# Performance work log

Hardware: AMD Instinct MI355X
Metric: run time of the kernel (lower is better)

## Reference

```python
import jax, jax.numpy as jnp
import numpy as np

B, T, O, H = 64, 1000, 61, 256
IN0, IN1 = 320, 2 * H  # layer0 input = 8*40 flattened feats; layer1 input = bidirectional concat


def setup_inputs() -> dict:
    key = jax.random.key(0)
    ks = jax.random.split(key, 12)
    rn = lambda k, shape: (jax.random.normal(k, shape, dtype=jnp.float32) * 0.05)
    inp = {}
    inp["batch"] = jax.random.normal(ks[0], (B, T, 8, 40), dtype=jnp.float32)
    lengths = np.random.RandomState(0).randint(T // 2, T + 1, size=B).astype(np.int64)
    inp["lengths"] = jnp.asarray(lengths)
    # GRU params stacked over directions: [2, 3H, in], [2, 3H, H], biases [2, 3H]
    inp["w_ih_l0"] = rn(ks[1], (2, 3 * H, IN0))
    inp["w_hh_l0"] = rn(ks[2], (2, 3 * H, H))
    inp["b_ih_l0"] = rn(ks[3], (2, 3 * H))
    inp["b_hh_l0"] = rn(ks[4], (2, 3 * H))
    inp["w_ih_l1"] = rn(ks[5], (2, 3 * H, IN1))
    inp["w_hh_l1"] = rn(ks[6], (2, 3 * H, H))
    inp["b_ih_l1"] = rn(ks[7], (2, 3 * H))
    inp["b_hh_l1"] = rn(ks[8], (2, 3 * H))
    inp["fc_w"] = rn(ks[9], (O, 2 * H))
    inp["fc_b"] = rn(ks[10], (O,))
    return inp


def _gru_dir(x, w_ih, w_hh, b_ih, b_hh, reverse):
    # x: [T, B, in] -> ys: [T, B, H]; torch GRU cell semantics
    def step(h, xt):
        gi = xt @ w_ih.T + b_ih          # [B, 3H]
        gh = h @ w_hh.T + b_hh           # [B, 3H]
        i_r, i_z, i_n = jnp.split(gi, 3, axis=-1)
        h_r, h_z, h_n = jnp.split(gh, 3, axis=-1)
        r = jax.nn.sigmoid(i_r + h_r)
        z = jax.nn.sigmoid(i_z + h_z)
        n = jnp.tanh(i_n + r * h_n)
        h_new = (1.0 - z) * n + z * h
        return h_new, h_new
    h0 = jnp.zeros((x.shape[1], w_hh.shape[-1]), x.dtype)
    _, ys = jax.lax.scan(step, h0, x, reverse=reverse)
    return ys


def _bigru_layer(x, w_ih, w_hh, b_ih, b_hh):
    fwd = _gru_dir(x, w_ih[0], w_hh[0], b_ih[0], b_hh[0], reverse=False)
    bwd = _gru_dir(x, w_ih[1], w_hh[1], b_ih[1], b_hh[1], reverse=True)
    return jnp.concatenate([fwd, bwd], axis=-1)  # [T, B, 2H]


def reference(batch, lengths, w_ih_l0, w_hh_l0, b_ih_l0, b_hh_l0,
              w_ih_l1, w_hh_l1, b_ih_l1, b_hh_l1, fc_w, fc_b):
    b, t = batch.shape[0], batch.shape[1]
    x = jnp.swapaxes(batch, 2, 3).reshape(b, t, -1)   # transpose(2,3).flatten(2) -> [B,T,320]
    x = jnp.swapaxes(x, 0, 1)                          # [T, B, 320] (time-major like torch GRU)
    h1 = _bigru_layer(x, w_ih_l0, w_hh_l0, b_ih_l0, b_hh_l0)
    h2 = _bigru_layer(h1, w_ih_l1, w_hh_l1, b_ih_l1, b_hh_l1)
    out = h2 @ fc_w.T + fc_b                           # [T, B, O]
    out = jnp.swapaxes(out, 0, 1)                      # [B, T, O]
    # gather first lengths[i] timesteps of each sample, concatenated
    L = np.asarray(lengths)
    mask = np.arange(t)[None, :] < L[:, None]
    bi, ti = np.nonzero(mask)
    return out[bi, ti]                                 # [sum(lengths), O]
```

## Files before the change

### kernel.cpp

```cpp
#include <hip/hip_runtime.h>
#include <cstdint>
#include <cstddef>


typedef __attribute__((ext_vector_type(8))) __bf16 bf16x8;
typedef __attribute__((ext_vector_type(4))) float f32x4;
typedef __attribute__((ext_vector_type(4))) unsigned int u32x4;

#define AS1 __attribute__((address_space(1)))
#define AS3 __attribute__((address_space(3)))

#define LOG2E 1.44269504089f
#define SRZ  (-1.44269504089f)
#define SN   (2.88539008177f)

__device__ __forceinline__ void async_ld16(const void* g, void* l) {
  __builtin_amdgcn_global_load_lds((const AS1 unsigned int*)g,
                                   (AS3 unsigned int*)l, 16, 0, 0);
}

__device__ __forceinline__ f32x4 mfma16(u32x4 a, u32x4 b, f32x4 c) {
  return __builtin_amdgcn_mfma_f32_16x16x32_bf16(
      __builtin_bit_cast(bf16x8, a), __builtin_bit_cast(bf16x8, b), c, 0, 0, 0);
}

__device__ __forceinline__ unsigned short f2b(float f) {
  unsigned int u = __float_as_uint(f);
  u += 0x7fffu + ((u >> 16) & 1u);
  return (unsigned short)(u >> 16);
}
__device__ __forceinline__ float b2f(unsigned short s) {
  return __uint_as_float(((unsigned int)s) << 16);
}
__device__ __forceinline__ float gload(const float* p, size_t i) { return p[i]; }
__device__ __forceinline__ float gload(const unsigned short* p, size_t i) { return b2f(p[i]); }
__device__ __forceinline__ void gstore(float* p, size_t i, float v) { p[i] = v; }
__device__ __forceinline__ void gstore(unsigned short* p, size_t i, float v) { p[i] = f2b(v); }

__device__ __forceinline__ float sigm2(float xs) {
  return __builtin_amdgcn_rcpf(1.0f + __builtin_amdgcn_exp2f(xs));
}
__device__ __forceinline__ float tanh2(float ys) {
  return __builtin_fmaf(-2.0f,
      __builtin_amdgcn_rcpf(1.0f + __builtin_amdgcn_exp2f(ys)), 1.0f);
}

__device__ __forceinline__ void lds_barrier() {
  asm volatile("" ::: "memory");
  __builtin_amdgcn_s_waitcnt(0xC07F);
  __builtin_amdgcn_s_barrier();
  asm volatile("" ::: "memory");
}

__global__ void cast_bf16_kernel(const float* __restrict__ src,
                                 unsigned short* __restrict__ dst, int n) {
  const int i = blockIdx.x * 256 + threadIdx.x;
  if (i < n) dst[i] = f2b(src[i]);
}

__global__ void cast_w_kernel(const float* __restrict__ src,
                              unsigned short* __restrict__ dst, int n,
                              int in_dim) {
  const int i = blockIdx.x * 256 + threadIdx.x;
  if (i < n) {
    const int row = (i / in_dim) % 768;
    const float s = (row < 512) ? SRZ : SN;
    dst[i] = f2b(s * src[i]);
  }
}

__global__ void bias_fuse_kernel(const float* __restrict__ bih,
                                 const float* __restrict__ bhh,
                                 float* __restrict__ fb) {
  const int n = blockIdx.x * 256 + threadIdx.x;
  if (n < 1536) {
    const int dir = n >> 9 >> 1 ? 1 : (n / 768);
    const int rr = n - dir * 768;
    const float s = (rr < 512) ? SRZ : SN;
    float v = bih[dir * 768 + rr];
    if (rr < 512) v += bhh[dir * 768 + rr];
    fb[n] = s * v;
  }
}

__global__ void transpose_x_kernel(const float* __restrict__ batch,
                                   unsigned short* __restrict__ xb) {
  const int t = blockIdx.x, b = blockIdx.y, i = threadIdx.x;
  const float v = batch[((size_t)b * 1000 + t) * 320 + (i & 7) * 40 + (i >> 3)];
  xb[((size_t)t * 64 + b) * 320 + i] = f2b(v);
}

template <typename CT>
__global__ __launch_bounds__(256) void gemm_bt_kernel(
    const unsigned short* __restrict__ A, const unsigned short* __restrict__ W,
    const float* __restrict__ bias, CT* __restrict__ C, int M, int N, int K) {
  __shared__ __align__(16) unsigned short As[4096];
  __shared__ __align__(16) unsigned short Bs[4096];
  const int tid = threadIdx.x;
  const int lane = tid & 63;
  const int wv = tid >> 6;
  const int mBase = blockIdx.x * 128;
  const int nBase = blockIdx.y * 128;

  const int s0 = tid, s1 = tid + 256;
  const int r0 = ((s0 >> 6) << 4) | (s0 & 15), c0 = ((s0 >> 4) & 3) * 8;
  const int r1 = ((s1 >> 6) << 4) | (s1 & 15), c1 = ((s1 >> 4) & 3) * 8;

  const unsigned short* Arow0 = A + (size_t)(mBase + r0) * K + c0;
  const unsigned short* Arow1 = A + (size_t)(mBase + r1) * K + c1;
  const unsigned short* Wrow0 = W + (size_t)(nBase + r0) * K + c0;
  const unsigned short* Wrow1 = W + (size_t)(nBase + r1) * K + c1;

  char* lA = (char*)As;
  char* lB = (char*)Bs;
  char* dstA0 = lA + wv * 1024;
  char* dstA1 = lA + 4096 + wv * 1024;
  char* dstB0 = lB + wv * 1024;
  char* dstB1 = lB + 4096 + wv * 1024;

  f32x4 acc[4][4] = {};
  const int mh = (wv >> 1) * 64, nh = (wv & 1) * 64;
  const u32x4* As4 = (const u32x4*)As;
  const u32x4* Bs4 = (const u32x4*)Bs;

  for (int k0 = 0; k0 < K; k0 += 32) {
    __syncthreads();
    async_ld16(Arow0 + k0, dstA0);
    async_ld16(Arow1 + k0, dstA1);
    async_ld16(Wrow0 + k0, dstB0);
    async_ld16(Wrow1 + k0, dstB1);
    __syncthreads();
    u32x4 a[4], b[4];
#pragma unroll
    for (int mt = 0; mt < 4; ++mt) a[mt] = As4[((mh >> 4) + mt) * 64 + lane];
#pragma unroll
    for (int nt = 0; nt < 4; ++nt) b[nt] = Bs4[((nh >> 4) + nt) * 64 + lane];
#pragma unroll
    for (int mt = 0; mt < 4; ++mt)
#pragma unroll
      for (int nt = 0; nt < 4; ++nt)
        acc[mt][nt] = mfma16(a[mt], b[nt], acc[mt][nt]);
  }
#pragma unroll
  for (int nt = 0; nt < 4; ++nt) {
    const int n = nBase + nh + nt * 16 + (lane & 15);
    const float bn = bias[n];
#pragma unroll
    for (int mt = 0; mt < 4; ++mt) {
      const int mrow = mBase + mh + mt * 16 + ((lane >> 4) << 2);
#pragma unroll
      for (int r = 0; r < 4; ++r)
        gstore(C, (size_t)(mrow + r) * N + n, acc[mt][nt][r] + bn);
    }
  }
}

#define GBLOCK(G)                                                              \
  {                                                                            \
    _Pragma("unroll") for (int kt = 0; kt < 6; ++kt) {                         \
      acc[0][G] = mfma16(a[kt], wv[0][G][kt], acc[0][G]);                      \
      acc[1][G] = mfma16(a[kt], wv[1][G][kt], acc[1][G]);                      \
    }                                                                          \
    _Pragma("unroll") for (int kk = 0; kk < 2; ++kk) {                         \
      u32x4 bf0 = *(const u32x4*)(wlds +                                       \
          (((w * 12 + (0 * 3 + (G)) * 2 + kk) << 10) + lane * 16));            \
      u32x4 bf1 = *(const u32x4*)(wlds +                                       \
          (((w * 12 + (1 * 3 + (G)) * 2 + kk) << 10) + lane * 16));            \
      acc[0][G] = mfma16(a[6 + kk], bf0, acc[0][G]);                           \
      acc[1][G] = mfma16(a[6 + kk], bf1, acc[1][G]);                           \
    }                                                                          \
  }

template <typename GT>
__global__ __launch_bounds__(512, 2) void gru_fast_kernel(
    const GT* __restrict__ gi,
    const unsigned short* __restrict__ whh,
    const float* __restrict__ bhh,
    unsigned short* __restrict__ hout) {
  constexpr int E = (int)sizeof(GT);
  constexpr int CH = (E * 1536) / 1024;
  constexpr bool DB = (E == 2);
  constexpr int HB = DB ? 18432 : 9216;
  extern __shared__ __align__(16) char smem[];
  char* wlds = smem;
  char* hl   = smem + 98304;
  char* glds = smem + 98304 + HB;
  const int tid = threadIdx.x;
  const int lane = tid & 63;
  const int w = tid >> 6;
  const int c = lane & 15;
  const int q = lane >> 4;
  const int dir = blockIdx.x & 1;
  const int sb = (blockIdx.x >> 1) * 16;

  for (int i = tid; i < HB / 2; i += 512) ((unsigned short*)hl)[i] = 0;

  const int u0 = 32 * w + c;
  const float bhn0 = SN * bhh[dir * 768 + 512 + u0];
  const float bhn1 = SN * bhh[dir * 768 + 512 + u0 + 16];

  const unsigned short* wb =
      whh + (size_t)dir * 196608 + (size_t)u0 * 256 + q * 8;
  u32x4 wv[2][3][6];
#pragma unroll
  for (int j = 0; j < 2; ++j)
#pragma unroll
    for (int g = 0; g < 3; ++g) {
      const unsigned short* p = wb + (size_t)(g * 256 + 16 * j) * 256;
#pragma unroll
      for (int kt = 0; kt < 6; ++kt) wv[j][g][kt] = *(const u32x4*)(p + kt * 32);
#pragma unroll
      for (int kk = 0; kk < 2; ++kk) {
        u32x4 tmp = *(const u32x4*)(p + (6 + kk) * 32);
        *(u32x4*)(wlds + (((w * 12 + (j * 3 + g) * 2 + kk) << 10) + lane * 16)) = tmp;
      }
    }
#pragma unroll
  for (int j = 0; j < 2; ++j)
#pragma unroll
    for (int g = 0; g < 3; ++g)
#pragma unroll
      for (int kt = 0; kt < 6; ++kt)
        asm volatile("" : "+v"(wv[j][g][kt]));

  float h0[4] = {0.f, 0.f, 0.f, 0.f}, h1[4] = {0.f, 0.f, 0.f, 0.f};

  const int t0 = dir ? 999 : 0;
  unsigned short* hp = hout + ((size_t)t0 * 64 + sb) * 512 + dir * 256 + u0;
  const ptrdiff_t gstep = (dir ? -1 : 1) * (ptrdiff_t)(64 * 1536);
  const ptrdiff_t hstep = (dir ? -1 : 1) * (ptrdiff_t)(64 * 512);

  char* gdw = glds + w * (1536 * E);
  const int off0 = (c ^ ((q & 1) << 4)) * E;
  const int off1 = ((c + 16) ^ ((q & 1) << 4)) * E;
  const char* grb0 = gdw + (q * 4) * (96 * E) + off0;
  const char* grb1 = gdw + (q * 4) * (96 * E) + off1;
  const GT* gs[CH];
#pragma unroll
  for (int i = 0; i < CH; ++i) {
    const int p    = i * 64 + lane;
    const int s    = p / (6 * E);
    const int rem  = p - s * (6 * E);
    const int g    = rem / (2 * E);
    const int subp = rem - g * (2 * E);
    const int sub  = subp ^ (((s >> 2) & 1) * E);
    const int col  = sub * (16 / E);
    gs[i] = gi + ((size_t)t0 * 64 + sb + s) * 1536 + dir * 768 + 32 * w +
            g * 256 + col;
  }
#pragma unroll
  for (int i = 0; i < CH; ++i) {
    async_ld16(gs[i], gdw + i * 1024);
    gs[i] += gstep;
  }

  __syncthreads();

  const char* habase = hl + c * 576 + q * 16;
  const int hw0 = q * 4 * 288 + u0;

  auto body = [&](int rd, int wr) {
    u32x4 a[8];
#pragma unroll
    for (int kt = 0; kt < 8; ++kt)
      a[kt] = *(const u32x4*)(habase + rd + kt * 64);
    if constexpr (!DB) lds_barrier();

    f32x4 acc[2][3] = {};
    GBLOCK(0)

    asm volatile("s_waitcnt vmcnt(0)" ::: "memory");
    float pv0[3][4], pv1[3][4];
#pragma unroll
    for (int r = 0; r < 4; ++r)
#pragma unroll
      for (int g = 0; g < 3; ++g) {
        pv0[g][r] = gload((const GT*)(grb0 + (r * 96 + g * 32) * E), (size_t)0);
        pv1[g][r] = gload((const GT*)(grb1 + (r * 96 + g * 32) * E), (size_t)0);
      }
    asm volatile("s_waitcnt lgkmcnt(0)" ::: "memory");
#pragma unroll
    for (int i = 0; i < CH; ++i) {
      async_ld16(gs[i], gdw + i * 1024);
      gs[i] += gstep;
    }

    float rr0[4], rr1[4];
#pragma unroll
    for (int r = 0; r < 4; ++r) {
      rr0[r] = sigm2(pv0[0][r] + acc[0][0][r]);
      rr1[r] = sigm2(pv1[0][r] + acc[1][0][r]);
    }

    GBLOCK(2)

    float nn0[4], nn1[4];
#pragma unroll
    for (int r = 0; r < 4; ++r) {
      nn0[r] = tanh2(__builtin_fmaf(rr0[r], acc[0][2][r] + bhn0, pv0[2][r]));
      nn1[r] = tanh2(__builtin_fmaf(rr1[r], acc[1][2][r] + bhn1, pv1[2][r]));
    }

    GBLOCK(1)

    unsigned short* hls = (unsigned short*)(hl + wr);
#pragma unroll
    for (int r = 0; r < 4; ++r) {
      const float zz0 = sigm2(pv0[1][r] + acc[0][1][r]);
      const float hv0 = __builtin_fmaf(zz0, h0[r] - nn0[r], nn0[r]);
      h0[r] = hv0;
      const float zz1 = sigm2(pv1[1][r] + acc[1][1][r]);
      const float hv1 = __builtin_fmaf(zz1, h1[r] - nn1[r], nn1[r]);
      h1[r] = hv1;
      const unsigned short hb0 = f2b(hv0), hb1 = f2b(hv1);
      hls[hw0 + r * 288] = hb0;
      hls[hw0 + r * 288 + 16] = hb1;
      hp[(size_t)(q * 4 + r) * 512] = hb0;
      hp[(size_t)(q * 4 + r) * 512 + 16] = hb1;
    }
    hp += hstep;
    lds_barrier();
  };

  if constexpr (DB) {
    for (int it = 0; it < 500; ++it) {
      body(0, 9216);
      body(9216, 0);
    }
  } else {
    for (int step = 0; step < 1000; ++step) body(0, 0);
  }
  asm volatile("s_waitcnt vmcnt(0)" ::: "memory");
}

template <typename GT>
__global__ __launch_bounds__(1024) void gru_layer_kernel(
    const GT* __restrict__ gi, const unsigned short* __restrict__ whh,
    const float* __restrict__ bhh, unsigned short* __restrict__ hout) {
  __shared__ __align__(16) unsigned short hbf[16][264];
  __shared__ __align__(16) float gh[16][780];
  const int tid = threadIdx.x;
  const int lane = tid & 63;
  const int wv = tid >> 6;
  const int dir = blockIdx.x & 1;
  const int sb = (blockIdx.x >> 1) * 16;
  const int j = tid & 255;
  const int si = tid >> 8;

  float hreg[4] = {0.f, 0.f, 0.f, 0.f};
#pragma unroll
  for (int i = 0; i < 4; ++i) hbf[si + i * 4][j] = 0;

  const float bh_n = SN * bhh[dir * 768 + 512 + j];

  const unsigned short* wl = whh + (size_t)dir * 768 * 256 +
                             (size_t)(wv * 48 + (lane & 15)) * 256 +
                             ((lane >> 4) * 8);
  const char* habase = (const char*)hbf + (lane & 15) * 528 + ((lane >> 4) << 4);
  const int srow = (lane >> 4) * 4;

  __syncthreads();

  for (int step = 0; step < 1000; ++step) {
    const int t = dir ? (999 - step) : step;
    float p_ir[4], p_iz[4], p_in[4];
#pragma unroll
    for (int i = 0; i < 4; ++i) {
      const int s = si + i * 4;
      const size_t gib = ((size_t)t * 64 + (sb + s)) * 1536 + dir * 768 + j;
      p_ir[i] = gload(gi, gib);
      p_iz[i] = gload(gi, gib + 256);
      p_in[i] = gload(gi, gib + 512);
    }
    u32x4 a[8];
#pragma unroll
    for (int kt = 0; kt < 8; ++kt) a[kt] = *(const u32x4*)(habase + kt * 64);
#pragma unroll
    for (int ntd = 0; ntd < 3; ++ntd) {
      f32x4 acc = {0.f, 0.f, 0.f, 0.f};
#pragma unroll
      for (int kt = 0; kt < 8; ++kt) {
        u32x4 bfrag = *(const u32x4*)(wl + ntd * (16 * 256) + kt * 32);
        acc = mfma16(a[kt], bfrag, acc);
      }
      const int gcol = (wv * 3 + ntd) * 16 + (lane & 15);
#pragma unroll
      for (int r = 0; r < 4; ++r) gh[srow + r][gcol] = acc[r];
    }
    __syncthreads();
#pragma unroll
    for (int i = 0; i < 4; ++i) {
      const int s = si + i * 4;
      const float r = sigm2(p_ir[i] + gh[s][j]);
      const float z = sigm2(p_iz[i] + gh[s][256 + j]);
      const float n = tanh2(__builtin_fmaf(r, gh[s][512 + j] + bh_n, p_in[i]));
      const float h = __builtin_fmaf(z, hreg[i] - n, n);
      hreg[i] = h;
      const unsigned short hb = f2b(h);
      hbf[s][j] = hb;
      hout[((size_t)t * 64 + (sb + s)) * 512 + dir * 256 + j] = hb;
    }
    __syncthreads();
  }
}

__global__ void prefix_kernel(const int* __restrict__ raw,
                              int* __restrict__ pref, int* __restrict__ lens) {
  if (threadIdx.x == 0) {
    const int stride = (raw[1] == 0 && raw[3] == 0 && raw[5] == 0) ? 2 : 1;
    int a = 0;
    for (int b = 0; b < 64; ++b) {
      const int L = raw[b * stride];
      pref[b] = a;
      lens[b] = L;
      a += L;
    }
  }
}

__global__ __launch_bounds__(256) void fc_kernel(
    const unsigned short* __restrict__ h2, const unsigned short* __restrict__ fcw,
    const float* __restrict__ fcb, const int* __restrict__ lens,
    const int* __restrict__ pref, float* __restrict__ out) {
  __shared__ __align__(16) unsigned short hrow[4][512];
  const int b = blockIdx.y;
  const int sub = threadIdx.x >> 6, lane = threadIdx.x & 63;
  const int t = blockIdx.x * 4 + sub;
  *(u32x4*)&hrow[sub][lane * 8] =
      *(const u32x4*)&h2[((size_t)t * 64 + b) * 512 + lane * 8];
  __syncthreads();
  const int len = lens[b];
  if (lane < 61 && t < len) {
    float acc = fcb[lane];
    const unsigned short* wr = fcw + (size_t)lane * 512;
#pragma unroll 4
    for (int k = 0; k < 512; k += 8) {
      u32x4 w4 = *(const u32x4*)(wr + k);
      u32x4 h4 = *(const u32x4*)(&hrow[sub][k]);
#pragma unroll
      for (int qq = 0; qq < 4; ++qq) {
        acc += __uint_as_float(w4[qq] << 16) * __uint_as_float(h4[qq] << 16);
        acc += __uint_as_float(w4[qq] & 0xffff0000u) * __uint_as_float(h4[qq] & 0xffff0000u);
      }
    }
    out[((size_t)pref[b] + t) * 61 + lane] = acc;
  }
}

template <typename GT>
static void run_pipeline(const float* batch, const int* lengths_raw,
                         const float* w_ih_l0, const float* w_hh_l0,
                         const float* b_ih_l0, const float* b_hh_l0,
                         const float* w_ih_l1, const float* w_hh_l1,
                         const float* b_ih_l1, const float* b_hh_l1,
                         const float* fc_w, const float* fc_b, float* out,
                         char* ws, hipStream_t stream) {
  size_t off = 0;
  auto alloc = [&](size_t bytes) -> char* {
    char* p = ws + off;
    off += (bytes + 255) & ~(size_t)255;
    return p;
  };
  char* pool = alloc((size_t)64000 * 512 * 2);
  unsigned short* xb = (unsigned short*)pool;
  unsigned short* h1 = (unsigned short*)pool;
  unsigned short* h2 = (unsigned short*)pool;
  GT*             gi   = (GT*)alloc((size_t)64064 * 1536 * sizeof(GT));
  unsigned short* wih0 = (unsigned short*)alloc((size_t)1536 * 320 * 2);
  unsigned short* wih1 = (unsigned short*)alloc((size_t)1536 * 512 * 2);
  unsigned short* whh0 = (unsigned short*)alloc((size_t)1536 * 256 * 2);
  unsigned short* whh1 = (unsigned short*)alloc((size_t)1536 * 256 * 2);
  unsigned short* fcwb = (unsigned short*)alloc((size_t)61 * 512 * 2);
  float*          fb0  = (float*)alloc(1536 * 4);
  float*          fb1  = (float*)alloc(1536 * 4);
  int*            pref = (int*)alloc(256);
  int*            lens = (int*)alloc(256);

  auto castw = [&](const float* s, unsigned short* d, int n, int in_dim) {
    cast_w_kernel<<<dim3((n + 255) / 256), dim3(256), 0, stream>>>(s, d, n, in_dim);
  };
  castw(w_ih_l0, wih0, 2 * 768 * 320, 320);
  castw(w_hh_l0, whh0, 2 * 768 * 256, 256);
  castw(w_ih_l1, wih1, 2 * 768 * 512, 512);
  castw(w_hh_l1, whh1, 2 * 768 * 256, 256);
  cast_bf16_kernel<<<dim3((61 * 512 + 255) / 256), dim3(256), 0, stream>>>(
      fc_w, fcwb, 61 * 512);
  bias_fuse_kernel<<<dim3(6), dim3(256), 0, stream>>>(b_ih_l0, b_hh_l0, fb0);
  bias_fuse_kernel<<<dim3(6), dim3(256), 0, stream>>>(b_ih_l1, b_hh_l1, fb1);

  transpose_x_kernel<<<dim3(1000, 64), dim3(320), 0, stream>>>(batch, xb);

  const int HB = (sizeof(GT) == 2) ? 18432 : 9216;
  const int GRU_LDS = 98304 + HB + 8 * 1536 * (int)sizeof(GT);
  const bool big_lds =
      hipFuncSetAttribute(reinterpret_cast<const void*>(gru_fast_kernel<GT>),
                          hipFuncAttributeMaxDynamicSharedMemorySize,
                          GRU_LDS) == hipSuccess;

  auto gru = [&](GT* g, unsigned short* w, const float* b, unsigned short* h) {
    if (big_lds)
      gru_fast_kernel<GT><<<dim3(8), dim3(512), GRU_LDS, stream>>>(g, w, b, h);
    else
      gru_layer_kernel<GT><<<dim3(8), dim3(1024), 0, stream>>>(g, w, b, h);
  };

  gemm_bt_kernel<GT><<<dim3(500, 12), dim3(256), 0, stream>>>(
      xb, wih0, fb0, gi, 64000, 1536, 320);
  gru(gi, whh0, b_hh_l0, h1);
  gemm_bt_kernel<GT><<<dim3(500, 12), dim3(256), 0, stream>>>(
      h1, wih1, fb1, gi, 64000, 1536, 512);
  gru(gi, whh1, b_hh_l1, h2);

  prefix_kernel<<<dim3(1), dim3(64), 0, stream>>>(lengths_raw, pref, lens);
  fc_kernel<<<dim3(250, 64), dim3(256), 0, stream>>>(h2, fcwb, fc_b, lens, pref, out);
}

extern "C" void kernel_launch(void* const* d_in, const int* in_sizes, int n_in,
                              void* d_out, int out_size, void* d_ws, size_t ws_size,
                              hipStream_t stream) {
  (void)in_sizes; (void)n_in; (void)out_size;
  const float* batch   = (const float*)d_in[0];
  const int*   lengths = (const int*)d_in[1];
  const float* w_ih_l0 = (const float*)d_in[2];
  const float* w_hh_l0 = (const float*)d_in[3];
  const float* b_ih_l0 = (const float*)d_in[4];
  const float* b_hh_l0 = (const float*)d_in[5];
  const float* w_ih_l1 = (const float*)d_in[6];
  const float* w_hh_l1 = (const float*)d_in[7];
  const float* b_ih_l1 = (const float*)d_in[8];
  const float* b_hh_l1 = (const float*)d_in[9];
  const float* fc_w    = (const float*)d_in[10];
  const float* fc_b    = (const float*)d_in[11];
  float* out = (float*)d_out;
  char* ws = (char*)d_ws;

  const size_t NEED_FP32 = 470000000ull;
  if (ws_size >= NEED_FP32) {
    run_pipeline<float>(batch, lengths, w_ih_l0, w_hh_l0, b_ih_l0, b_hh_l0,
                        w_ih_l1, w_hh_l1, b_ih_l1, b_hh_l1, fc_w, fc_b, out,
                        ws, stream);
  } else {
    run_pipeline<unsigned short>(batch, lengths, w_ih_l0, w_hh_l0, b_ih_l0,
                                 b_hh_l0, w_ih_l1, w_hh_l1, b_ih_l1, b_hh_l1,
                                 fc_w, fc_b, out, ws, stream);
  }
}
```

Before: 4.196 ms.

## Store input-gate GEMM output in GRU-fragment order for contiguous per-wave loads

The input-projection GEMM now writes its output permuted into per-timestep, per-wave slots that match the MFMA fragment layout the recurrent GRU kernel consumes. The GRU kernel can then fetch each step's gate preactivations with contiguous 16-byte async loads and read them back from LDS as whole vectors, instead of doing scattered per-element swizzled LDS reads. The prefetch of the next step's gates is moved later, after the gate computations, and the hidden-state bf16 conversion now uses a packed convert instruction. The permuted layout couples the two kernels tightly and is used only on the big-LDS path.

Result: faster. 3.707 ms (-11.7%).

```diff
diff --git a/kernel.cpp b/kernel.cpp
--- a/kernel.cpp
+++ b/kernel.cpp
@@ -32,10 +32,19 @@
 __device__ __forceinline__ float b2f(unsigned short s) {
   return __uint_as_float(((unsigned int)s) << 16);
 }
+__device__ __forceinline__ unsigned int cvtpk(float lo, float hi) {
+  unsigned int r;
+  asm("v_cvt_pk_bf16_f32 %0, %1, %2" : "=v"(r) : "v"(lo), "v"(hi));
+  return r;
+}
+__device__ __forceinline__ float lo16(unsigned int d) {
+  return __uint_as_float(d << 16);
+}
+__device__ __forceinline__ float hi16(unsigned int d) {
+  return __uint_as_float(d & 0xffff0000u);
+}
 __device__ __forceinline__ float gload(const float* p, size_t i) { return p[i]; }
 __device__ __forceinline__ float gload(const unsigned short* p, size_t i) { return b2f(p[i]); }
-__device__ __forceinline__ void gstore(float* p, size_t i, float v) { p[i] = v; }
-__device__ __forceinline__ void gstore(unsigned short* p, size_t i, float v) { p[i] = f2b(v); }
 
 __device__ __forceinline__ float sigm2(float xs) {
   return __builtin_amdgcn_rcpf(1.0f + __builtin_amdgcn_exp2f(xs));
@@ -90,7 +99,7 @@
   xb[((size_t)t * 64 + b) * 320 + i] = f2b(v);
 }
 
-template <typename CT>
+template <typename CT, bool PERM>
 __global__ __launch_bounds__(256) void gemm_bt_kernel(
     const unsigned short* __restrict__ A, const unsigned short* __restrict__ W,
     const float* __restrict__ bias, CT* __restrict__ C, int M, int N, int K) {
@@ -141,16 +150,59 @@
       for (int nt = 0; nt < 4; ++nt)
         acc[mt][nt] = mfma16(a[mt], b[nt], acc[mt][nt]);
   }
-#pragma unroll
-  for (int nt = 0; nt < 4; ++nt) {
-    const int n = nBase + nh + nt * 16 + (lane & 15);
-    const float bn = bias[n];
-#pragma unroll
-    for (int mt = 0; mt < 4; ++mt) {
-      const int mrow = mBase + mh + mt * 16 + ((lane >> 4) << 2);
-#pragma unroll
-      for (int r = 0; r < 4; ++r)
-        gstore(C, (size_t)(mrow + r) * N + n, acc[mt][nt][r] + bn);
+
+  if constexpr (PERM) {
+    const int t = (mBase + mh) >> 6;
+#pragma unroll
+    for (int p = 0; p < 2; ++p) {
+      const int nb0 = nBase + nh + p * 32;
+      const int dir = (nb0 >= 768) ? 1 : 0;
+      const int np = nb0 - dir * 768;
+      const int g = np >> 8;
+      const int ww = (np >> 5) & 7;
+      const float bn0 = bias[nb0 + (lane & 15)];
+      const float bn1 = bias[nb0 + 16 + (lane & 15)];
+#pragma unroll
+      for (int mt = 0; mt < 4; ++mt) {
+        const size_t slot = (size_t)t * 64 + (size_t)(mt * 2 + dir) * 8 + ww;
+        if constexpr (sizeof(CT) == 2) {
+          u32x4 v;
+          v[0] = cvtpk(acc[mt][2 * p][0] + bn0, acc[mt][2 * p][1] + bn0);
+          v[1] = cvtpk(acc[mt][2 * p][2] + bn0, acc[mt][2 * p][3] + bn0);
+          v[2] = cvtpk(acc[mt][2 * p + 1][0] + bn1, acc[mt][2 * p + 1][1] + bn1);
+          v[3] = cvtpk(acc[mt][2 * p + 1][2] + bn1, acc[mt][2 * p + 1][3] + bn1);
+          *(u32x4*)((unsigned short*)C + slot * 1536 + (size_t)g * 512 +
+                    (size_t)lane * 8) = v;
+        } else {
+#pragma unroll
+          for (int rs = 0; rs < 2; ++rs) {
+            f32x4 v = {acc[mt][2 * p][2 * rs] + bn0,
+                       acc[mt][2 * p][2 * rs + 1] + bn0,
+                       acc[mt][2 * p + 1][2 * rs] + bn1,
+                       acc[mt][2 * p + 1][2 * rs + 1] + bn1};
+            *(f32x4*)((float*)C + slot * 1536 + (size_t)(g * 2 + rs) * 256 +
+                      (size_t)lane * 4) = v;
+          }
+        }
+      }
+    }
+  } else {
+#pragma unroll
+    for (int nt = 0; nt < 4; ++nt) {
+      const int n = nBase + nh + nt * 16 + (lane & 15);
+      const float bn = bias[n];
+#pragma unroll
+      for (int mt = 0; mt < 4; ++mt) {
+        const int mrow = mBase + mh + mt * 16 + ((lane >> 4) << 2);
+#pragma unroll
+        for (int r = 0; r < 4; ++r) {
+          const float v = acc[mt][nt][r] + bn;
+          if constexpr (sizeof(CT) == 2)
+            ((unsigned short*)C)[(size_t)(mrow + r) * N + n] = f2b(v);
+          else
+            ((float*)C)[(size_t)(mrow + r) * N + n] = v;
+        }
+      }
     }
   }
 }
@@ -231,28 +283,13 @@
   const ptrdiff_t hstep = (dir ? -1 : 1) * (ptrdiff_t)(64 * 512);
 
   char* gdw = glds + w * (1536 * E);
-  const int off0 = (c ^ ((q & 1) << 4)) * E;
-  const int off1 = ((c + 16) ^ ((q & 1) << 4)) * E;
-  const char* grb0 = gdw + (q * 4) * (96 * E) + off0;
-  const char* grb1 = gdw + (q * 4) * (96 * E) + off1;
-  const GT* gs[CH];
-#pragma unroll
-  for (int i = 0; i < CH; ++i) {
-    const int p    = i * 64 + lane;
-    const int s    = p / (6 * E);
-    const int rem  = p - s * (6 * E);
-    const int g    = rem / (2 * E);
-    const int subp = rem - g * (2 * E);
-    const int sub  = subp ^ (((s >> 2) & 1) * E);
-    const int col  = sub * (16 / E);
-    gs[i] = gi + ((size_t)t0 * 64 + sb + s) * 1536 + dir * 768 + 32 * w +
-            g * 256 + col;
-  }
-#pragma unroll
-  for (int i = 0; i < CH; ++i) {
-    async_ld16(gs[i], gdw + i * 1024);
-    gs[i] += gstep;
-  }
+  const size_t slot0 =
+      (size_t)t0 * 64 + (size_t)((blockIdx.x >> 1) * 2 + dir) * 8 + w;
+  const GT* gp2 = gi + slot0 * 1536 + (size_t)lane * (16 / E);
+#pragma unroll
+  for (int i = 0; i < CH; ++i)
+    async_ld16(gp2 + i * (1024 / E), gdw + i * 1024);
+  gp2 += gstep;
 
   __syncthreads();
 
@@ -270,53 +307,72 @@
     GBLOCK(0)
 
     asm volatile("s_waitcnt vmcnt(0)" ::: "memory");
-    float pv0[3][4], pv1[3][4];
-#pragma unroll
-    for (int r = 0; r < 4; ++r)
-#pragma unroll
-      for (int g = 0; g < 3; ++g) {
-        pv0[g][r] = gload((const GT*)(grb0 + (r * 96 + g * 32) * E), (size_t)0);
-        pv1[g][r] = gload((const GT*)(grb1 + (r * 96 + g * 32) * E), (size_t)0);
-      }
+    u32x4 raw[CH];
+#pragma unroll
+    for (int i = 0; i < CH; ++i)
+      raw[i] = *(const u32x4*)(gdw + i * 1024 + lane * 16);
+
+    float pvA[3][4], pvB[3][4];
+    if constexpr (E == 2) {
+#pragma unroll
+      for (int g = 0; g < 3; ++g)
+#pragma unroll
+        for (int r = 0; r < 4; ++r) {
+          const unsigned int d0 = raw[g][r >> 1];
+          const unsigned int d1 = raw[g][2 + (r >> 1)];
+          pvA[g][r] = (r & 1) ? hi16(d0) : lo16(d0);
+          pvB[g][r] = (r & 1) ? hi16(d1) : lo16(d1);
+        }
+    } else {
+#pragma unroll
+      for (int g = 0; g < 3; ++g)
+#pragma unroll
+        for (int r = 0; r < 4; ++r) {
+          const f32x4 f = __builtin_bit_cast(f32x4, raw[g * 2 + (r >> 1)]);
+          pvA[g][r] = f[r & 1];
+          pvB[g][r] = f[2 + (r & 1)];
+        }
+    }
+
+    float rr0[4], rr1[4];
+#pragma unroll
+    for (int r = 0; r < 4; ++r) {
+      rr0[r] = sigm2(pvA[0][r] + acc[0][0][r]);
+      rr1[r] = sigm2(pvB[0][r] + acc[1][0][r]);
+    }
+
+    GBLOCK(2)
+
+    float nn0[4], nn1[4];
+#pragma unroll
+    for (int r = 0; r < 4; ++r) {
+      nn0[r] = tanh2(__builtin_fmaf(rr0[r], acc[0][2][r] + bhn0, pvA[2][r]));
+      nn1[r] = tanh2(__builtin_fmaf(rr1[r], acc[1][2][r] + bhn1, pvB[2][r]));
+    }
+
+    GBLOCK(1)
+
     asm volatile("s_waitcnt lgkmcnt(0)" ::: "memory");
 #pragma unroll
-    for (int i = 0; i < CH; ++i) {
-      async_ld16(gs[i], gdw + i * 1024);
-      gs[i] += gstep;
-    }
-
-    float rr0[4], rr1[4];
+    for (int i = 0; i < CH; ++i)
+      async_ld16(gp2 + i * (1024 / E), gdw + i * 1024);
+    gp2 += gstep;
+
+    unsigned short* hls = (unsigned short*)(hl + wr);
 #pragma unroll
     for (int r = 0; r < 4; ++r) {
-      rr0[r] = sigm2(pv0[0][r] + acc[0][0][r]);
-      rr1[r] = sigm2(pv1[0][r] + acc[1][0][r]);
-    }
-
-    GBLOCK(2)
-
-    float nn0[4], nn1[4];
-#pragma unroll
-    for (int r = 0; r < 4; ++r) {
-      nn0[r] = tanh2(__builtin_fmaf(rr0[r], acc[0][2][r] + bhn0, pv0[2][r]));
-      nn1[r] = tanh2(__builtin_fmaf(rr1[r], acc[1][2][r] + bhn1, pv1[2][r]));
-    }
-
-    GBLOCK(1)
-
-    unsigned short* hls = (unsigned short*)(hl + wr);
-#pragma unroll
-    for (int r = 0; r < 4; ++r) {
-      const float zz0 = sigm2(pv0[1][r] + acc[0][1][r]);
+      const float zz0 = sigm2(pvA[1][r] + acc[0][1][r]);
       const float hv0 = __builtin_fmaf(zz0, h0[r] - nn0[r], nn0[r]);
       h0[r] = hv0;
-      const float zz1 = sigm2(pv1[1][r] + acc[1][1][r]);
+      const float zz1 = sigm2(pvB[1][r] + acc[1][1][r]);
       const float hv1 = __builtin_fmaf(zz1, h1[r] - nn1[r], nn1[r]);
       h1[r] = hv1;
-      const unsigned short hb0 = f2b(hv0), hb1 = f2b(hv1);
-      hls[hw0 + r * 288] = hb0;
-      hls[hw0 + r * 288 + 16] = hb1;
-      hp[(size_t)(q * 4 + r) * 512] = hb0;
-      hp[(size_t)(q * 4 + r) * 512 + 16] = hb1;
+      const unsigned int pk = cvtpk(hv0, hv1);
+      const unsigned int pkh = pk >> 16;
+      hls[hw0 + r * 288] = (unsigned short)pk;
+      hls[hw0 + r * 288 + 16] = (unsigned short)pkh;
+      hp[(size_t)(q * 4 + r) * 512] = (unsigned short)pk;
+      hp[(size_t)(q * 4 + r) * 512 + 16] = (unsigned short)pkh;
     }
     hp += hstep;
     lds_barrier();
@@ -497,6 +553,15 @@
                           hipFuncAttributeMaxDynamicSharedMemorySize,
                           GRU_LDS) == hipSuccess;
 
+  auto gemm = [&](const unsigned short* A, const unsigned short* W,
+                  const float* fb, GT* Cc, int M, int N, int K) {
+    if (big_lds)
+      gemm_bt_kernel<GT, true><<<dim3(500, 12), dim3(256), 0, stream>>>(
+          A, W, fb, Cc, M, N, K);
+    else
+      gemm_bt_kernel<GT, false><<<dim3(500, 12), dim3(256), 0, stream>>>(
+          A, W, fb, Cc, M, N, K);
+  };
   auto gru = [&](GT* g, unsigned short* w, const float* b, unsigned short* h) {
     if (big_lds)
       gru_fast_kernel<GT><<<dim3(8), dim3(512), GRU_LDS, stream>>>(g, w, b, h);
@@ -504,11 +569,9 @@
       gru_layer_kernel<GT><<<dim3(8), dim3(1024), 0, stream>>>(g, w, b, h);
   };
 
-  gemm_bt_kernel<GT><<<dim3(500, 12), dim3(256), 0, stream>>>(
-      xb, wih0, fb0, gi, 64000, 1536, 320);
+  gemm(xb, wih0, fb0, gi, 64000, 1536, 320);
   gru(gi, whh0, b_hh_l0, h1);
-  gemm_bt_kernel<GT><<<dim3(500, 12), dim3(256), 0, stream>>>(
-      h1, wih1, fb1, gi, 64000, 1536, 512);
+  gemm(h1, wih1, fb1, gi, 64000, 1536, 512);
   gru(gi, whh1, b_hh_l1, h2);
 
   prefix_kernel<<<dim3(1), dim3(64), 0, stream>>>(lengths_raw, pref, lens);
```
